# Optimization experiments

Hardware: AMD Instinct MI355X
Metric: run time of the kernel (lower is better)

Reference implementation:

```python
import jax, jax.numpy as jnp
import numpy as np

B, S, H = 1, 2048, 2048
E, K, I = 8, 2, 1024   # n_routed_experts, num_experts_per_tok, moe_intermediate_size
IS = 2 * I             # shared experts intermediate = moe_intermediate_size * n_shared_experts


def setup_inputs() -> dict:
    key = jax.random.key(0)
    ks = jax.random.split(key, 8)
    w = 0.02  # weight scale so gate softmax is not degenerate
    return {
        "x": jax.random.normal(ks[0], (B, S, H), jnp.float32),
        "gate_w": jax.random.normal(ks[1], (E, H), jnp.float32) * w,
        "wg": jax.random.normal(ks[2], (E, H, I), jnp.float32) * w,
        "wu": jax.random.normal(ks[3], (E, H, I), jnp.float32) * w,
        "wd": jax.random.normal(ks[4], (E, I, H), jnp.float32) * w,
        "sg": jax.random.normal(ks[5], (H, IS), jnp.float32) * w,
        "su": jax.random.normal(ks[6], (H, IS), jnp.float32) * w,
        "sd": jax.random.normal(ks[7], (IS, H), jnp.float32) * w,
    }


def reference(x, gate_w, wg, wu, wd, sg, su, sd):
    b, s, h = x.shape
    xf = x.reshape(-1, h)                                  # [T, H]
    T = xf.shape[0]

    # ---- gate: softmax scores, top-k, renormalize ----
    scores = jax.nn.softmax(jnp.einsum("th,eh->te", xf, gate_w), axis=-1)  # [T, E]
    topk_w, topk_i = jax.lax.top_k(scores, K)              # sorted descending
    topk_w = topk_w / jnp.sum(topk_w, axis=-1, keepdims=True)

    # dense combine weights [T, E] (indices unique per token)
    cw = jnp.zeros_like(scores).at[jnp.arange(T)[:, None], topk_i].add(topk_w)

    # ---- routed experts: SwiGLU MLP per expert, weighted combine ----
    g = jnp.einsum("th,ehi->eti", xf, wg)                  # [E, T, I]
    u = jnp.einsum("th,ehi->eti", xf, wu)
    hgated = jax.nn.silu(g) * u
    eo = jnp.einsum("eti,eih->eth", hgated, wd)            # [E, T, H]
    y = jnp.einsum("te,eth->th", cw, eo)                   # [T, H]

    # ---- shared experts ----
    shared = (jax.nn.silu(xf @ sg) * (xf @ su)) @ sd       # [T, H]

    return (y + shared).reshape(b, s, h)
```

## Files before the change

kernel.cpp:

```cpp
#include <hip/hip_runtime.h>


typedef unsigned short u16;
typedef unsigned int   u32;
typedef __bf16 bf16x8 __attribute__((ext_vector_type(8)));
typedef float  f32x4  __attribute__((ext_vector_type(4)));

#define T_TOK 2048
#define HDIM  2048
#define IDIM  1024
#define NEXP  8
#define ISDIM 2048
#define MAXROWS   5760
#define MAXROWS_FB 5120

__device__ __forceinline__ u16 f2bf(float f) {
  u32 x = __float_as_uint(f);
  return (u16)((x + 0x7FFFu + ((x >> 16) & 1u)) >> 16);
}
__device__ __forceinline__ float bf2f(u16 v) { return __uint_as_float(((u32)v) << 16); }

#define GLL(g, l)                                                              \
  __builtin_amdgcn_global_load_lds(                                            \
      (const __attribute__((address_space(1))) void*)(g),                      \
      (__attribute__((address_space(3))) void*)(l), 16, 0, 0)

__global__ void init_kernel(int* __restrict__ perm, int* __restrict__ meta,
                            int* __restrict__ zrow) {
  int idx = blockIdx.x * 256 + threadIdx.x;
  if (idx < 8192) perm[idx] = -1;
  if (idx < 16) meta[idx] = 0;
  if (idx < 1024) zrow[idx] = 0;
}

__global__ __launch_bounds__(256) void gate_kernel(
    const float* __restrict__ x, const float* __restrict__ gw,
    u16* __restrict__ xb, float* __restrict__ outz,
    float* __restrict__ topw, int* __restrict__ topi, int* __restrict__ meta) {
  const int t = blockIdx.x, tid = threadIdx.x;
  const long o = (long)t * HDIM + tid * 8;
  float4 a = *(const float4*)(x + o);
  float4 b = *(const float4*)(x + o + 4);
  float4 z = {0.f, 0.f, 0.f, 0.f};
  *(float4*)(outz + o) = z;
  *(float4*)(outz + o + 4) = z;
  uint4 w;
  w.x = (u32)f2bf(a.x) | ((u32)f2bf(a.y) << 16);
  w.y = (u32)f2bf(a.z) | ((u32)f2bf(a.w) << 16);
  w.z = (u32)f2bf(b.x) | ((u32)f2bf(b.y) << 16);
  w.w = (u32)f2bf(b.z) | ((u32)f2bf(b.w) << 16);
  *(uint4*)(xb + o) = w;
  float acc[NEXP];
#pragma unroll
  for (int e = 0; e < NEXP; e++) {
    const float* gr = gw + e * HDIM + tid * 8;
    float4 wa = *(const float4*)gr;
    float4 wb = *(const float4*)(gr + 4);
    acc[e] = a.x * wa.x + a.y * wa.y + a.z * wa.z + a.w * wa.w +
             b.x * wb.x + b.y * wb.y + b.z * wb.z + b.w * wb.w;
  }
#pragma unroll
  for (int off = 32; off; off >>= 1)
#pragma unroll
    for (int e = 0; e < NEXP; e++) acc[e] += __shfl_down(acc[e], off, 64);
  __shared__ float red[4][NEXP];
  if ((tid & 63) == 0) {
#pragma unroll
    for (int e = 0; e < NEXP; e++) red[tid >> 6][e] = acc[e];
  }
  __syncthreads();
  if (tid == 0) {
    float s[NEXP];
#pragma unroll
    for (int e = 0; e < NEXP; e++) s[e] = red[0][e] + red[1][e] + red[2][e] + red[3][e];
    int i0 = 0;
#pragma unroll
    for (int e = 1; e < NEXP; e++)
      if (s[e] > s[i0]) i0 = e;
    int i1 = -1;
#pragma unroll
    for (int e = 0; e < NEXP; e++) {
      if (e == i0) continue;
      if (i1 < 0 || s[e] > s[i1]) i1 = e;
    }
    float w0 = 1.f / (1.f + __expf(s[i1] - s[i0]));
    topw[t * 2 + 0] = w0;
    topw[t * 2 + 1] = 1.f - w0;
    topi[t * 2 + 0] = i0;
    topi[t * 2 + 1] = i1;
    atomicAdd(meta + i0, 1);
    atomicAdd(meta + i1, 1);
  }
}

__global__ void scan_kernel(int* __restrict__ meta, int pad) {
  if (threadIdx.x == 0 && blockIdx.x == 0) {
    int o = 0;
    meta[16] = 0;
#pragma unroll
    for (int e = 0; e < NEXP; e++) {
      o += ((meta[e] + pad - 1) / pad) * pad;
      meta[17 + e] = o;
    }
  }
}

__global__ void assign_kernel(const int* __restrict__ topi, int* __restrict__ meta,
                              int* __restrict__ perm, int* __restrict__ tokrow) {
  int idx = blockIdx.x * 256 + threadIdx.x;
  int e = topi[idx];
  int pos = atomicAdd(meta + 8 + e, 1);
  int row = meta[16 + e] + pos;
  perm[row] = idx;
  tokrow[idx] = row;
}

__device__ __forceinline__ void tcast_tile(const float* __restrict__ in,
                                           u16* __restrict__ out, int R, int C) {
  __shared__ float tile[64 * 65];
  int r0 = blockIdx.y * 64, c0 = blockIdx.x * 64;
  int t = threadIdx.x;
  int i = t >> 4, j4 = t & 15;
#pragma unroll
  for (int ii = 0; ii < 4; ii++) {
    int r = i + ii * 16;
    float4 v = *(const float4*)(in + (long)(r0 + r) * C + c0 + j4 * 4);
    tile[r * 65 + j4 * 4 + 0] = v.x;
    tile[r * 65 + j4 * 4 + 1] = v.y;
    tile[r * 65 + j4 * 4 + 2] = v.z;
    tile[r * 65 + j4 * 4 + 3] = v.w;
  }
  __syncthreads();
  int cc = t >> 3, rr = (t & 7) * 8;
#pragma unroll
  for (int pp = 0; pp < 2; pp++) {
    int c = cc + pp * 32;
    u16 e[8];
#pragma unroll
    for (int u = 0; u < 8; u++) e[u] = f2bf(tile[(rr + u) * 65 + c]);
    uint4 w;
    w.x = (u32)e[0] | ((u32)e[1] << 16);
    w.y = (u32)e[2] | ((u32)e[3] << 16);
    w.z = (u32)e[4] | ((u32)e[5] << 16);
    w.w = (u32)e[6] | ((u32)e[7] << 16);
    *(uint4*)(out + (long)(c0 + c) * R + r0 + rr) = w;
  }
}

__global__ __launch_bounds__(256) void tcast_kernel(const float* __restrict__ in,
                                                    u16* __restrict__ out, int R, int C,
                                                    long inz, long outz) {
  tcast_tile(in + (long)blockIdx.z * inz, out + (long)blockIdx.z * outz, R, C);
}

__global__ __launch_bounds__(256) void tcast2_kernel(
    const float* __restrict__ inA, const float* __restrict__ inB,
    u16* __restrict__ out, int R, int C, long inz, long outz, long boff, int zsplit) {
  int z = blockIdx.z;
  const float* in;
  u16* o;
  if (z < zsplit) {
    in = inA + (long)z * inz;
    o = out + (long)z * outz;
  } else {
    int e = z - zsplit;
    in = inB + (long)e * inz;
    o = out + (long)e * outz + boff;
  }
  tcast_tile(in, o, R, C);
}

template <int HALF8>
__device__ __forceinline__ void silu_do(u16* __restrict__ buf, long i) {
  long r = i / HALF8, c = i % HALF8;
  u16* g = buf + r * (long)HALF8 * 16 + c * 8;
  uint4 gv = *(const uint4*)g;
  uint4 uv = *(const uint4*)(g + HALF8 * 8);
  const u32* gp = &gv.x;
  const u32* up = &uv.x;
  uint4 w;
  u32* wp = &w.x;
#pragma unroll
  for (int j = 0; j < 4; j++) {
    float g0 = bf2f((u16)(gp[j] & 0xFFFF)), g1 = bf2f((u16)(gp[j] >> 16));
    float u0 = bf2f((u16)(up[j] & 0xFFFF)), u1 = bf2f((u16)(up[j] >> 16));
    float r0 = g0 / (1.f + __expf(-g0)) * u0;
    float r1 = g1 / (1.f + __expf(-g1)) * u1;
    wp[j] = (u32)f2bf(r0) | ((u32)f2bf(r1) << 16);
  }
  *(uint4*)g = w;
}

template <int HALF8>
__global__ void silu_kernel(u16* __restrict__ buf) {
  long i = (long)blockIdx.x * 256 + threadIdx.x;
  silu_do<HALF8>(buf, i);
}

__global__ void silu2_kernel(u16* __restrict__ gur, u16* __restrict__ gus) {
  const long NR = (long)MAXROWS * IDIM / 8;
  long i = (long)blockIdx.x * 256 + threadIdx.x;
  if (i < NR)
    silu_do<128>(gur, i);
  else
    silu_do<256>(gus, i - NR);
}

template <int CMODE , int MI, bool PERMA, bool SEGB>
__device__ __forceinline__ void gemm_body3(
    int mt, int nt, u16* lds, const u16* __restrict__ A, long lda,
    const u16* __restrict__ B, long ldbz, int K, u16* __restrict__ Cb,
    float* __restrict__ Cf, long ldc, const int* __restrict__ offp,
    const int* __restrict__ perm, const u16* __restrict__ zrow) {
  const int row0 = mt * (MI * 32);
  if constexpr (SEGB) {
    if (row0 >= offp[8]) return;
    int e = 0;
    while (offp[e + 1] <= row0) ++e;
    B += (long)e * ldbz;
  }
  const int tid = threadIdx.x;

  const int ra = tid >> 2, sa = tid & 3;
  const int swz0 = (sa ^ ((ra >> 1) & 3)) * 8;
  const u16 *gA0, *gA1;
  if constexpr (PERMA) {
    int p0 = perm[row0 + ra];
    int p1 = perm[row0 + 128 + ra];
    gA0 = ((p0 < 0) ? zrow : A + (long)(p0 >> 1) * lda) + swz0;
    gA1 = ((p1 < 0) ? zrow : A + (long)(p1 >> 1) * lda) + swz0;
  } else {
    gA0 = A + (long)(row0 + ra) * lda + swz0;
    gA1 = A + (long)(row0 + 128 + ra) * lda + swz0;
  }
  const u16* gB0 = B + (long)(nt * 256 + ra) * K + swz0;
  const u16* gB1 = B + (long)(nt * 256 + 128 + ra) * K + swz0;

  const int lane = tid & 63, w = tid >> 6;
  const int wm = (w >> 2) * (MI * 16), wn = (w & 3) * 64;
  const int lrow = lane & 15, kc = lane >> 4;
  int offA[MI], offB[4];
#pragma unroll
  for (int i = 0; i < MI; i++) {
    int r = wm + i * 16 + lrow;
    offA[i] = r * 32 + ((kc ^ ((r >> 1) & 3)) << 3);
  }
#pragma unroll
  for (int i = 0; i < 4; i++) {
    int r = wn + i * 16 + lrow;
    offB[i] = 8192 + r * 32 + ((kc ^ ((r >> 1) & 3)) << 3);
  }

  f32x4 acc[MI][4];
#pragma unroll
  for (int i = 0; i < MI; i++)
#pragma unroll
    for (int j = 0; j < 4; j++) acc[i][j] = f32x4{0.f, 0.f, 0.f, 0.f};

  const int nk = K >> 5;
  {
    u16* b0 = lds;
    GLL(gA0, b0 + tid * 8);
    GLL(gA1, b0 + 4096 + tid * 8);
    GLL(gB0, b0 + 8192 + tid * 8);
    GLL(gB1, b0 + 12288 + tid * 8);
    u16* b1 = lds + 16384;
    GLL(gA0 + 32, b1 + tid * 8);
    GLL(gA1 + 32, b1 + 4096 + tid * 8);
    GLL(gB0 + 32, b1 + 8192 + tid * 8);
    GLL(gB1 + 32, b1 + 12288 + tid * 8);
  }
  asm volatile("s_waitcnt vmcnt(4)" ::: "memory");
  asm volatile("s_barrier" ::: "memory");

  constexpr int MH = MI / 2;
  int cur = 0, stg = 2;
  for (int t = 0; t < nk; ++t) {
    int t2 = t + 2;
    if (t2 >= nk) t2 -= nk;
    const int kk2 = t2 * 32;
    u16* buf = lds + cur * 16384;
    u16* sb = lds + stg * 16384;

    bf16x8 af[MH], bfv[4];
#pragma unroll
    for (int i = 0; i < MH; i++) af[i] = *(const bf16x8*)(buf + offA[i]);
#pragma unroll
    for (int i = 0; i < 4; i++) bfv[i] = *(const bf16x8*)(buf + offB[i]);
    GLL(gA0 + kk2, sb + tid * 8);
    GLL(gA1 + kk2, sb + 4096 + tid * 8);
    asm volatile("s_barrier" ::: "memory");
    __builtin_amdgcn_s_setprio(1);
#pragma unroll
    for (int mi = 0; mi < MH; mi++)
#pragma unroll
      for (int ni = 0; ni < 4; ni++)
        acc[mi][ni] = __builtin_amdgcn_mfma_f32_16x16x32_bf16(af[mi], bfv[ni],
                                                              acc[mi][ni], 0, 0, 0);
    __builtin_amdgcn_s_setprio(0);
    asm volatile("s_barrier" ::: "memory");

    bf16x8 ag[MI - MH];
#pragma unroll
    for (int i = 0; i < MI - MH; i++) ag[i] = *(const bf16x8*)(buf + offA[MH + i]);
    GLL(gB0 + kk2, sb + 8192 + tid * 8);
    GLL(gB1 + kk2, sb + 12288 + tid * 8);
    asm volatile("s_barrier" ::: "memory");
    __builtin_amdgcn_s_setprio(1);
#pragma unroll
    for (int mi = 0; mi < MI - MH; mi++)
#pragma unroll
      for (int ni = 0; ni < 4; ni++)
        acc[MH + mi][ni] = __builtin_amdgcn_mfma_f32_16x16x32_bf16(
            ag[mi], bfv[ni], acc[MH + mi][ni], 0, 0, 0);
    __builtin_amdgcn_s_setprio(0);
    asm volatile("s_waitcnt vmcnt(4)" ::: "memory");
    asm volatile("s_barrier" ::: "memory");
    cur = (cur == 2) ? 0 : cur + 1;
    stg = (stg == 2) ? 0 : stg + 1;
  }
  asm volatile("s_waitcnt vmcnt(0)" ::: "memory");

  const int crow = row0 + wm + ((lane >> 4) << 2);
  const int ccol = nt * 256 + wn + (lane & 15);
#pragma unroll
  for (int mi = 0; mi < MI; mi++) {
#pragma unroll
    for (int ni = 0; ni < 4; ni++) {
#pragma unroll
      for (int r = 0; r < 4; r++) {
        int row = crow + mi * 16 + r;
        int col = ccol + ni * 16;
        float v = acc[mi][ni][r];
        if constexpr (CMODE == 0) {
          Cb[(long)row * ldc + col] = f2bf(v);
        } else {
          Cf[(long)row * ldc + col] = v;
        }
      }
    }
  }
}

__global__ __launch_bounds__(512, 2) void gemm_gu_fused(
    const u16* __restrict__ xb, const u16* __restrict__ wguT,
    const u16* __restrict__ sgsuT, u16* __restrict__ gur, u16* __restrict__ gus,
    const int* __restrict__ offp, const int* __restrict__ perm,
    const u16* __restrict__ zrow) {
  __shared__ __align__(16) u16 lds3[49152];
  int bid = blockIdx.x;
  if (bid < 128) {
    gemm_body3<0, 8, false, false>(bid >> 4, bid & 15, lds3, xb, HDIM, sgsuT, 0, HDIM,
                                   gus, nullptr, 2 * ISDIM, nullptr, nullptr, nullptr);
  } else {
    int b = bid - 128;
    gemm_body3<0, 6, true, true>(b >> 3, b & 7, lds3, xb, HDIM, wguT,
                                 (long)2 * IDIM * HDIM, HDIM, gur, nullptr, 2 * IDIM,
                                 offp, perm, zrow);
  }
}

__global__ __launch_bounds__(512, 2) void gemm_down_plain(
    const u16* __restrict__ gus, const u16* __restrict__ sdT,
    const u16* __restrict__ gur, const u16* __restrict__ wdT, float* __restrict__ out,
    u16* __restrict__ eo, const int* __restrict__ offp) {
  __shared__ __align__(16) u16 lds3[49152];
  int bid = blockIdx.x;
  if (bid < 64) {
    gemm_body3<1, 8, false, false>(bid >> 3, bid & 7, lds3, gus, 2 * ISDIM, sdT, 0,
                                   ISDIM, nullptr, out, HDIM, nullptr, nullptr, nullptr);
  } else {
    int b = bid - 64;
    gemm_body3<0, 6, false, true>(b >> 3, b & 7, lds3, gur, 2 * IDIM, wdT,
                                  (long)HDIM * IDIM, IDIM, eo, nullptr, HDIM, offp,
                                  nullptr, nullptr);
  }
}

__global__ __launch_bounds__(256) void combine_kernel(float* __restrict__ out,
                                                      const u16* __restrict__ eo,
                                                      const int* __restrict__ tokrow,
                                                      const float* __restrict__ topw) {
  const int t = blockIdx.x, tid = threadIdx.x;
  const long o = (long)t * HDIM + tid * 8;
  const int r0 = tokrow[t * 2], r1 = tokrow[t * 2 + 1];
  const float w0 = topw[t * 2], w1 = topw[t * 2 + 1];
  float4 a = *(const float4*)(out + o);
  float4 b = *(const float4*)(out + o + 4);
  uint4 e0 = *(const uint4*)(eo + (long)r0 * HDIM + tid * 8);
  uint4 e1 = *(const uint4*)(eo + (long)r1 * HDIM + tid * 8);
  const u32* p0 = &e0.x;
  const u32* p1 = &e1.x;
  float r[8] = {a.x, a.y, a.z, a.w, b.x, b.y, b.z, b.w};
#pragma unroll
  for (int j = 0; j < 4; j++) {
    r[j * 2 + 0] += w0 * bf2f((u16)(p0[j] & 0xFFFF)) + w1 * bf2f((u16)(p1[j] & 0xFFFF));
    r[j * 2 + 1] += w0 * bf2f((u16)(p0[j] >> 16)) + w1 * bf2f((u16)(p1[j] >> 16));
  }
  float4 oa = {r[0], r[1], r[2], r[3]};
  float4 ob = {r[4], r[5], r[6], r[7]};
  *(float4*)(out + o) = oa;
  *(float4*)(out + o + 4) = ob;
}

template <int CMODE, bool PERMA, bool SEGB>
__device__ __forceinline__ void gemm_body(
    int mt, int nt, u16* ldsA, u16* ldsB, const u16* __restrict__ A, long lda,
    const u16* __restrict__ B, long ldbz, int K, u16* __restrict__ Cb,
    float* __restrict__ Cf, long ldc, const int* __restrict__ offp,
    const int* __restrict__ perm, const float* __restrict__ topw,
    const u16* __restrict__ zrow) {
  const int row0 = mt * 128;
  if constexpr (SEGB) {
    if (row0 >= offp[8]) return;
    int e = 0;
    while (offp[e + 1] <= row0) ++e;
    B += (long)e * ldbz;
  }
  const int tid = threadIdx.x;
  const u16* gA[4];
  const u16* gB[4];
  u16 *lA[4], *lB[4];
#pragma unroll
  for (int j = 0; j < 4; j++) {
    int c = tid + 256 * j;
    int r = c >> 3, s = c & 7;
    int gk = (s ^ (r & 7)) * 8;
    const u16* arow;
    if constexpr (PERMA) {
      int p = perm[row0 + r];
      arow = (p < 0) ? zrow : A + (long)(p >> 1) * lda;
    } else {
      arow = A + (long)(row0 + r) * lda;
    }
    gA[j] = arow + gk;
    gB[j] = B + (long)(nt * 128 + r) * K + gk;
    lA[j] = ldsA + c * 8;
    lB[j] = ldsB + c * 8;
  }
  const int lane = tid & 63, wave = tid >> 6;
  const int wm = (wave & 1) * 64, wn = (wave >> 1) * 64;
  const int lrow = lane & 15;
  const int kchunk = lane >> 4;
  const int rsw = lrow & 7;

  f32x4 acc[4][4];
#pragma unroll
  for (int i = 0; i < 4; i++)
#pragma unroll
    for (int j = 0; j < 4; j++) acc[i][j] = f32x4{0.f, 0.f, 0.f, 0.f};

  const int nk = K >> 6;
  for (int kt = 0; kt < nk; ++kt) {
    const int kk = kt * 64;
#pragma unroll
    for (int j = 0; j < 4; j++) {
      GLL(gA[j] + kk, lA[j]);
      GLL(gB[j] + kk, lB[j]);
    }
    __syncthreads();
#pragma unroll
    for (int half = 0; half < 2; half++) {
      const int slot = (kchunk + half * 4) ^ rsw;
      bf16x8 af[4], bfv[4];
#pragma unroll
      for (int mi = 0; mi < 4; mi++)
        af[mi] = *(const bf16x8*)(ldsA + (wm + lrow + mi * 16) * 64 + slot * 8);
#pragma unroll
      for (int ni = 0; ni < 4; ni++)
        bfv[ni] = *(const bf16x8*)(ldsB + (wn + lrow + ni * 16) * 64 + slot * 8);
#pragma unroll
      for (int mi = 0; mi < 4; mi++)
#pragma unroll
        for (int ni = 0; ni < 4; ni++)
          acc[mi][ni] = __builtin_amdgcn_mfma_f32_16x16x32_bf16(af[mi], bfv[ni],
                                                                acc[mi][ni], 0, 0, 0);
    }
    __syncthreads();
  }

  const int crow = row0 + wm + ((lane >> 4) << 2);
  const int ccol = nt * 128 + wn + (lane & 15);
#pragma unroll
  for (int mi = 0; mi < 4; mi++) {
#pragma unroll
    for (int ni = 0; ni < 4; ni++) {
#pragma unroll
      for (int r = 0; r < 4; r++) {
        int row = crow + mi * 16 + r;
        int col = ccol + ni * 16;
        float v = acc[mi][ni][r];
        if constexpr (CMODE == 0) {
          Cb[(long)row * ldc + col] = f2bf(v);
        } else if constexpr (CMODE == 1) {
          Cf[(long)row * ldc + col] = v;
        } else if constexpr (CMODE == 2) {
          int p = perm[row];
          if (p >= 0) atomicAdd(Cf + (long)(p >> 1) * ldc + col, topw[p] * v);
        } else {
          atomicAdd(Cf + (long)row * ldc + col, v);
        }
      }
    }
  }
}

__global__ __launch_bounds__(256) void gemm_routed_gu(
    const u16* __restrict__ xb, const u16* __restrict__ wT, u16* __restrict__ Cb,
    const int* __restrict__ offp, const int* __restrict__ perm,
    const u16* __restrict__ zrow) {
  __shared__ __align__(16) u16 ldsA[8192], ldsB[8192];
  gemm_body<0, true, true>(blockIdx.y, blockIdx.x, ldsA, ldsB, xb, HDIM, wT,
                           (long)IDIM * HDIM, HDIM, Cb, nullptr, 2 * IDIM, offp, perm,
                           nullptr, zrow);
}
__global__ __launch_bounds__(256) void gemm_shared_gu(const u16* __restrict__ xb,
                                                      const u16* __restrict__ sgsuT,
                                                      u16* __restrict__ gus) {
  __shared__ __align__(16) u16 ldsA[8192], ldsB[8192];
  gemm_body<0, false, false>(blockIdx.y, blockIdx.x, ldsA, ldsB, xb, HDIM, sgsuT, 0, HDIM,
                             gus, nullptr, 2 * ISDIM, nullptr, nullptr, nullptr, nullptr);
}
__global__ __launch_bounds__(256) void gemm_down_atomic(
    const u16* __restrict__ gus, const u16* __restrict__ sdT,
    const u16* __restrict__ gur, const u16* __restrict__ wdT, float* __restrict__ out,
    const int* __restrict__ offp, const int* __restrict__ perm,
    const float* __restrict__ topw) {
  __shared__ __align__(16) u16 ldsA[8192], ldsB[8192];
  int bid = blockIdx.x;
  if (bid < 256) {
    gemm_body<3, false, false>(bid / 16, bid % 16, ldsA, ldsB, gus, 2 * ISDIM, sdT, 0,
                               ISDIM, nullptr, out, HDIM, nullptr, nullptr, nullptr,
                               nullptr);
  } else {
    int b = bid - 256;
    gemm_body<2, false, true>(b / 16, b % 16, ldsA, ldsB, gur, 2 * IDIM, wdT,
                              (long)HDIM * IDIM, IDIM, nullptr, out, HDIM, offp, perm,
                              topw, nullptr);
  }
}

extern "C" void kernel_launch(void* const* d_in, const int* in_sizes, int n_in,
                              void* d_out, int out_size, void* d_ws, size_t ws_size,
                              hipStream_t stream) {
  const float* x  = (const float*)d_in[0];
  const float* gw = (const float*)d_in[1];
  const float* wg = (const float*)d_in[2];
  const float* wu = (const float*)d_in[3];
  const float* wd = (const float*)d_in[4];
  const float* sg = (const float*)d_in[5];
  const float* su = (const float*)d_in[6];
  const float* sd = (const float*)d_in[7];
  float* out = (float*)d_out;

  char* ws = (char*)d_ws;
  size_t off = 0;
  auto alloc = [&](size_t b) {
    size_t o = off;
    off += (b + 255) & ~(size_t)255;
    return (void*)(ws + o);
  };
  u16*   xb     = (u16*)alloc((size_t)T_TOK * HDIM * 2);
  u16*   gur    = (u16*)alloc((size_t)MAXROWS * 2 * IDIM * 2);
  u16*   gus    = (u16*)alloc((size_t)T_TOK * 2 * ISDIM * 2);
  float* topw   = (float*)alloc((size_t)T_TOK * 2 * 4);
  int*   topi   = (int*)alloc((size_t)T_TOK * 2 * 4);
  int*   tokrow = (int*)alloc((size_t)T_TOK * 2 * 4);
  int*   perm   = (int*)alloc(8192 * 4);
  int*   meta   = (int*)alloc(64 * 4);
  u16*   zrow   = (u16*)alloc(4096);
  size_t base = off;

  const size_t SZ_WGUT  = (size_t)NEXP * 2 * IDIM * HDIM * 2;
  const size_t SZ_SGSUT = (size_t)2 * ISDIM * HDIM * 2;
  const size_t SZ_SDT   = (size_t)HDIM * ISDIM * 2;
  const size_t SZ_WDT   = (size_t)NEXP * HDIM * IDIM * 2;
  const bool fused = ws_size >= base + SZ_WGUT + SZ_SGSUT;

  init_kernel<<<32, 256, 0, stream>>>(perm, meta, (int*)zrow);
  gate_kernel<<<T_TOK, 256, 0, stream>>>(x, gw, xb, out, topw, topi, meta);
  scan_kernel<<<1, 64, 0, stream>>>(meta, fused ? 192 : 128);
  assign_kernel<<<16, 256, 0, stream>>>(topi, meta, perm, tokrow);

  if (fused) {
    u16* wguT  = (u16*)(ws + base);
    u16* sgsuT = (u16*)(ws + base + SZ_WGUT);
    u16* sdT   = wguT;
    u16* wdT   = wguT + SZ_SDT / 2;
    u16* eo    = wguT + (SZ_SDT + SZ_WDT) / 2;
    tcast2_kernel<<<dim3(IDIM / 64, HDIM / 64, 2 * NEXP), 256, 0, stream>>>(
        wg, wu, wguT, HDIM, IDIM, (long)HDIM * IDIM, (long)2 * IDIM * HDIM,
        (long)IDIM * HDIM, NEXP);
    tcast2_kernel<<<dim3(ISDIM / 64, HDIM / 64, 2), 256, 0, stream>>>(
        sg, su, sgsuT, HDIM, ISDIM, 0, 0, (long)ISDIM * HDIM, 1);
    gemm_gu_fused<<<368, 512, 0, stream>>>(xb, wguT, sgsuT, gur, gus, meta + 16, perm,
                                           zrow);
    silu2_kernel<<<(MAXROWS * IDIM / 8 + T_TOK * ISDIM / 8) / 256, 256, 0, stream>>>(
        gur, gus);
    tcast_kernel<<<dim3(HDIM / 64, ISDIM / 64, 1), 256, 0, stream>>>(sd, sdT, ISDIM,
                                                                     HDIM, 0, 0);
    tcast_kernel<<<dim3(HDIM / 64, IDIM / 64, NEXP), 256, 0, stream>>>(
        wd, wdT, IDIM, HDIM, (long)IDIM * HDIM, (long)HDIM * IDIM);
    gemm_down_plain<<<304, 512, 0, stream>>>(gus, sdT, gur, wdT, out, eo, meta + 16);
    combine_kernel<<<T_TOK, 256, 0, stream>>>(out, eo, tokrow, topw);
  } else {
    u16* wT    = (u16*)(ws + base);
    u16* sgsuT = wT;
    u16* sdT   = wT;
    u16* wdT   = wT + SZ_SDT / 2;
    tcast_kernel<<<dim3(IDIM / 64, HDIM / 64, NEXP), 256, 0, stream>>>(
        wg, wT, HDIM, IDIM, (long)HDIM * IDIM, (long)IDIM * HDIM);
    gemm_routed_gu<<<dim3(8, MAXROWS_FB / 128), 256, 0, stream>>>(xb, wT, gur, meta + 16,
                                                                  perm, zrow);
    tcast_kernel<<<dim3(IDIM / 64, HDIM / 64, NEXP), 256, 0, stream>>>(
        wu, wT, HDIM, IDIM, (long)HDIM * IDIM, (long)IDIM * HDIM);
    gemm_routed_gu<<<dim3(8, MAXROWS_FB / 128), 256, 0, stream>>>(
        xb, wT, gur + IDIM, meta + 16, perm, zrow);
    silu_kernel<128><<<(MAXROWS_FB * IDIM / 8) / 256, 256, 0, stream>>>(gur);
    tcast_kernel<<<dim3(ISDIM / 64, HDIM / 64, 1), 256, 0, stream>>>(sg, sgsuT, HDIM,
                                                                     ISDIM, 0, 0);
    tcast_kernel<<<dim3(ISDIM / 64, HDIM / 64, 1), 256, 0, stream>>>(
        su, sgsuT + (size_t)ISDIM * HDIM, HDIM, ISDIM, 0, 0);
    gemm_shared_gu<<<dim3(32, 16), 256, 0, stream>>>(xb, sgsuT, gus);
    silu_kernel<256><<<(T_TOK * ISDIM / 8) / 256, 256, 0, stream>>>(gus);
    tcast_kernel<<<dim3(HDIM / 64, ISDIM / 64, 1), 256, 0, stream>>>(sd, sdT, ISDIM,
                                                                     HDIM, 0, 0);
    tcast_kernel<<<dim3(HDIM / 64, IDIM / 64, NEXP), 256, 0, stream>>>(
        wd, wdT, IDIM, HDIM, (long)IDIM * HDIM, (long)HDIM * IDIM);
    gemm_down_atomic<<<896, 256, 0, stream>>>(gus, sdT, gur, wdT, out, meta + 16, perm,
                                              topw);
  }
}
```

Before: 511.4 us.

## Fuse SiLU into gate/up GEMM epilogue and merge setup kernels

The gate/up weight transposes now interleave gate and up columns in 16-wide groups, so each GEMM tile holds matching g and u accumulators. SiLU(g)*u is then computed in the epilogue and written at half width, which removes the separate SiLU pass and halves the intermediate buffer traffic. Init and both up-projection transposes are merged into one front kernel. The scan is folded into the gate kernel through a last-block ticket, and the down-weight transposes are merged into one launch. This cuts launch count and memory traffic, but the ticket scan adds fence and atomic ordering risk.

```diff
diff --git a/kernel.cpp b/kernel.cpp
--- a/kernel.cpp
+++ b/kernel.cpp
@@ -29,14 +29,96 @@
                             int* __restrict__ zrow) {
   int idx = blockIdx.x * 256 + threadIdx.x;
   if (idx < 8192) perm[idx] = -1;
-  if (idx < 16) meta[idx] = 0;
+  if (idx < 32) meta[idx] = 0;
   if (idx < 1024) zrow[idx] = 0;
+}
+
+__device__ __forceinline__ void tcast_tile2(const float* __restrict__ in,
+                                            u16* __restrict__ out, int R, int C,
+                                            int r0, int c0, int ilv, int uoff) {
+  __shared__ float tile[64 * 65];
+  int t = threadIdx.x;
+  int i = t >> 4, j4 = t & 15;
+#pragma unroll
+  for (int ii = 0; ii < 4; ii++) {
+    int r = i + ii * 16;
+    float4 v = *(const float4*)(in + (long)(r0 + r) * C + c0 + j4 * 4);
+    tile[r * 65 + j4 * 4 + 0] = v.x;
+    tile[r * 65 + j4 * 4 + 1] = v.y;
+    tile[r * 65 + j4 * 4 + 2] = v.z;
+    tile[r * 65 + j4 * 4 + 3] = v.w;
+  }
+  __syncthreads();
+  int cc = t >> 3, rr = (t & 7) * 8;
+#pragma unroll
+  for (int pp = 0; pp < 2; pp++) {
+    int c = cc + pp * 32;
+    u16 e[8];
+#pragma unroll
+    for (int u = 0; u < 8; u++) e[u] = f2bf(tile[(rr + u) * 65 + c]);
+    uint4 w;
+    w.x = (u32)e[0] | ((u32)e[1] << 16);
+    w.y = (u32)e[2] | ((u32)e[3] << 16);
+    w.z = (u32)e[4] | ((u32)e[5] << 16);
+    w.w = (u32)e[6] | ((u32)e[7] << 16);
+    int cg = c0 + c;
+    int orow = ilv ? ((cg >> 4) << 5) + (cg & 15) + uoff : cg;
+    *(uint4*)(out + (long)orow * R + r0 + rr) = w;
+  }
+}
+
+__global__ __launch_bounds__(256) void front_kernel(
+    const float* __restrict__ wg, const float* __restrict__ wu,
+    const float* __restrict__ sg, const float* __restrict__ su,
+    u16* __restrict__ wguT, u16* __restrict__ sgsuT, int* __restrict__ perm,
+    int* __restrict__ meta, int* __restrict__ zrow) {
+  int b = blockIdx.x;
+  if (b >= 10240) {
+    int ib = b - 10240;
+    int idx = ib * 256 + threadIdx.x;
+    if (idx < 8192) perm[idx] = -1;
+    if (ib == 32) {
+      if (threadIdx.x < 32) meta[threadIdx.x] = 0;
+#pragma unroll
+      for (int k = 0; k < 4; k++) zrow[threadIdx.x * 4 + k] = 0;
+    }
+    return;
+  }
+  if (b < 8192) {
+    int z = b >> 9, rem = b & 511, y = rem >> 4, xk = rem & 15;
+    int isU = z >= 8 ? 1 : 0;
+    int e = isU ? z - 8 : z;
+    const float* in = (isU ? wu : wg) + (long)e * HDIM * IDIM;
+    u16* o = wguT + (long)e * 2 * IDIM * HDIM;
+    tcast_tile2(in, o, HDIM, IDIM, y * 64, xk * 64, 1, isU ? 16 : 0);
+  } else {
+    int b2 = b - 8192;
+    int z = b2 >> 10, rem = b2 & 1023, y = rem >> 5, xk = rem & 31;
+    const float* in = z ? su : sg;
+    tcast_tile2(in, sgsuT, HDIM, ISDIM, y * 64, xk * 64, 1, z ? 16 : 0);
+  }
+}
+
+__global__ __launch_bounds__(256) void tcast_back(const float* __restrict__ sd,
+                                                  const float* __restrict__ wd,
+                                                  u16* __restrict__ sdT,
+                                                  u16* __restrict__ wdT) {
+  int b = blockIdx.x;
+  if (b < 1024) {
+    int y = b >> 5, xk = b & 31;
+    tcast_tile2(sd, sdT, ISDIM, HDIM, y * 64, xk * 64, 0, 0);
+  } else {
+    int b2 = b - 1024;
+    int z = b2 >> 9, rem = b2 & 511, y = rem >> 5, xk = rem & 31;
+    tcast_tile2(wd + (long)z * IDIM * HDIM, wdT + (long)z * HDIM * IDIM, IDIM, HDIM,
+                y * 64, xk * 64, 0, 0);
+  }
 }
 
 __global__ __launch_bounds__(256) void gate_kernel(
     const float* __restrict__ x, const float* __restrict__ gw,
     u16* __restrict__ xb, float* __restrict__ outz,
-    float* __restrict__ topw, int* __restrict__ topi, int* __restrict__ meta) {
+    float* __restrict__ topw, int* __restrict__ topi, int* __restrict__ meta, int pad) {
   const int t = blockIdx.x, tid = threadIdx.x;
   const long o = (long)t * HDIM + tid * 8;
   float4 a = *(const float4*)(x + o);
@@ -90,6 +172,20 @@
     topi[t * 2 + 1] = i1;
     atomicAdd(meta + i0, 1);
     atomicAdd(meta + i1, 1);
+    if (pad > 0) {
+      __threadfence();
+      int ticket = atomicAdd(meta + 25, 1);
+      if (ticket == (int)gridDim.x - 1) {
+        int o2 = 0;
+        meta[16] = 0;
+#pragma unroll
+        for (int e = 0; e < NEXP; e++) {
+          int cnt = atomicAdd(meta + e, 0);
+          o2 += ((cnt + pad - 1) / pad) * pad;
+          meta[17 + e] = o2;
+        }
+      }
+    }
   }
 }
 
@@ -117,57 +213,12 @@
 
 __device__ __forceinline__ void tcast_tile(const float* __restrict__ in,
                                            u16* __restrict__ out, int R, int C) {
-  __shared__ float tile[64 * 65];
-  int r0 = blockIdx.y * 64, c0 = blockIdx.x * 64;
-  int t = threadIdx.x;
-  int i = t >> 4, j4 = t & 15;
-#pragma unroll
-  for (int ii = 0; ii < 4; ii++) {
-    int r = i + ii * 16;
-    float4 v = *(const float4*)(in + (long)(r0 + r) * C + c0 + j4 * 4);
-    tile[r * 65 + j4 * 4 + 0] = v.x;
-    tile[r * 65 + j4 * 4 + 1] = v.y;
-    tile[r * 65 + j4 * 4 + 2] = v.z;
-    tile[r * 65 + j4 * 4 + 3] = v.w;
-  }
-  __syncthreads();
-  int cc = t >> 3, rr = (t & 7) * 8;
-#pragma unroll
-  for (int pp = 0; pp < 2; pp++) {
-    int c = cc + pp * 32;
-    u16 e[8];
-#pragma unroll
-    for (int u = 0; u < 8; u++) e[u] = f2bf(tile[(rr + u) * 65 + c]);
-    uint4 w;
-    w.x = (u32)e[0] | ((u32)e[1] << 16);
-    w.y = (u32)e[2] | ((u32)e[3] << 16);
-    w.z = (u32)e[4] | ((u32)e[5] << 16);
-    w.w = (u32)e[6] | ((u32)e[7] << 16);
-    *(uint4*)(out + (long)(c0 + c) * R + r0 + rr) = w;
-  }
-}
-
+  tcast_tile2(in, out, R, C, blockIdx.y * 64, blockIdx.x * 64, 0, 0);
+}
 __global__ __launch_bounds__(256) void tcast_kernel(const float* __restrict__ in,
                                                     u16* __restrict__ out, int R, int C,
                                                     long inz, long outz) {
   tcast_tile(in + (long)blockIdx.z * inz, out + (long)blockIdx.z * outz, R, C);
-}
-
-__global__ __launch_bounds__(256) void tcast2_kernel(
-    const float* __restrict__ inA, const float* __restrict__ inB,
-    u16* __restrict__ out, int R, int C, long inz, long outz, long boff, int zsplit) {
-  int z = blockIdx.z;
-  const float* in;
-  u16* o;
-  if (z < zsplit) {
-    in = inA + (long)z * inz;
-    o = out + (long)z * outz;
-  } else {
-    int e = z - zsplit;
-    in = inB + (long)e * inz;
-    o = out + (long)e * outz + boff;
-  }
-  tcast_tile(in, o, R, C);
 }
 
 template <int HALF8>
@@ -190,23 +241,13 @@
   }
   *(uint4*)g = w;
 }
-
 template <int HALF8>
 __global__ void silu_kernel(u16* __restrict__ buf) {
   long i = (long)blockIdx.x * 256 + threadIdx.x;
   silu_do<HALF8>(buf, i);
 }
 
-__global__ void silu2_kernel(u16* __restrict__ gur, u16* __restrict__ gus) {
-  const long NR = (long)MAXROWS * IDIM / 8;
-  long i = (long)blockIdx.x * 256 + threadIdx.x;
-  if (i < NR)
-    silu_do<128>(gur, i);
-  else
-    silu_do<256>(gus, i - NR);
-}
-
-template <int CMODE , int MI, bool PERMA, bool SEGB>
+template <int EPI, int MI, bool PERMA, bool SEGB>
 __device__ __forceinline__ void gemm_body3(
     int mt, int nt, u16* lds, const u16* __restrict__ A, long lda,
     const u16* __restrict__ B, long ldbz, int K, u16* __restrict__ Cb,
@@ -322,20 +363,34 @@
   asm volatile("s_waitcnt vmcnt(0)" ::: "memory");
 
   const int crow = row0 + wm + ((lane >> 4) << 2);
-  const int ccol = nt * 256 + wn + (lane & 15);
 #pragma unroll
   for (int mi = 0; mi < MI; mi++) {
-#pragma unroll
-    for (int ni = 0; ni < 4; ni++) {
-#pragma unroll
-      for (int r = 0; r < 4; r++) {
-        int row = crow + mi * 16 + r;
-        int col = ccol + ni * 16;
-        float v = acc[mi][ni][r];
-        if constexpr (CMODE == 0) {
-          Cb[(long)row * ldc + col] = f2bf(v);
-        } else {
-          Cf[(long)row * ldc + col] = v;
+    if constexpr (EPI == 2) {
+      const int ccl = nt * 128 + (wn >> 1) + (lane & 15);
+#pragma unroll
+      for (int nh = 0; nh < 2; nh++) {
+        f32x4 g = acc[mi][nh * 2], u = acc[mi][nh * 2 + 1];
+#pragma unroll
+        for (int r = 0; r < 4; r++) {
+          float gg = g[r];
+          float h = gg / (1.f + __expf(-gg)) * u[r];
+          Cb[(long)(crow + mi * 16 + r) * ldc + ccl + nh * 16] = f2bf(h);
+        }
+      }
+    } else {
+      const int ccol = nt * 256 + wn + (lane & 15);
+#pragma unroll
+      for (int ni = 0; ni < 4; ni++) {
+#pragma unroll
+        for (int r = 0; r < 4; r++) {
+          int row = crow + mi * 16 + r;
+          int col = ccol + ni * 16;
+          float v = acc[mi][ni][r];
+          if constexpr (EPI == 0) {
+            Cb[(long)row * ldc + col] = f2bf(v);
+          } else {
+            Cf[(long)row * ldc + col] = v;
+          }
         }
       }
     }
@@ -350,12 +405,12 @@
   __shared__ __align__(16) u16 lds3[49152];
   int bid = blockIdx.x;
   if (bid < 128) {
-    gemm_body3<0, 8, false, false>(bid >> 4, bid & 15, lds3, xb, HDIM, sgsuT, 0, HDIM,
-                                   gus, nullptr, 2 * ISDIM, nullptr, nullptr, nullptr);
+    gemm_body3<2, 8, false, false>(bid >> 4, bid & 15, lds3, xb, HDIM, sgsuT, 0, HDIM,
+                                   gus, nullptr, ISDIM, nullptr, nullptr, nullptr);
   } else {
     int b = bid - 128;
-    gemm_body3<0, 6, true, true>(b >> 3, b & 7, lds3, xb, HDIM, wguT,
-                                 (long)2 * IDIM * HDIM, HDIM, gur, nullptr, 2 * IDIM,
+    gemm_body3<2, 6, true, true>(b >> 3, b & 7, lds3, xb, HDIM, wguT,
+                                 (long)2 * IDIM * HDIM, HDIM, gur, nullptr, IDIM,
                                  offp, perm, zrow);
   }
 }
@@ -367,11 +422,11 @@
   __shared__ __align__(16) u16 lds3[49152];
   int bid = blockIdx.x;
   if (bid < 64) {
-    gemm_body3<1, 8, false, false>(bid >> 3, bid & 7, lds3, gus, 2 * ISDIM, sdT, 0,
+    gemm_body3<1, 8, false, false>(bid >> 3, bid & 7, lds3, gus, ISDIM, sdT, 0,
                                    ISDIM, nullptr, out, HDIM, nullptr, nullptr, nullptr);
   } else {
     int b = bid - 64;
-    gemm_body3<0, 6, false, true>(b >> 3, b & 7, lds3, gur, 2 * IDIM, wdT,
+    gemm_body3<0, 6, false, true>(b >> 3, b & 7, lds3, gur, IDIM, wdT,
                                   (long)HDIM * IDIM, IDIM, eo, nullptr, HDIM, offp,
                                   nullptr, nullptr);
   }
@@ -577,30 +632,19 @@
   const size_t SZ_WDT   = (size_t)NEXP * HDIM * IDIM * 2;
   const bool fused = ws_size >= base + SZ_WGUT + SZ_SGSUT;
 
-  init_kernel<<<32, 256, 0, stream>>>(perm, meta, (int*)zrow);
-  gate_kernel<<<T_TOK, 256, 0, stream>>>(x, gw, xb, out, topw, topi, meta);
-  scan_kernel<<<1, 64, 0, stream>>>(meta, fused ? 192 : 128);
-  assign_kernel<<<16, 256, 0, stream>>>(topi, meta, perm, tokrow);
-
   if (fused) {
     u16* wguT  = (u16*)(ws + base);
     u16* sgsuT = (u16*)(ws + base + SZ_WGUT);
     u16* sdT   = wguT;
     u16* wdT   = wguT + SZ_SDT / 2;
     u16* eo    = wguT + (SZ_SDT + SZ_WDT) / 2;
-    tcast2_kernel<<<dim3(IDIM / 64, HDIM / 64, 2 * NEXP), 256, 0, stream>>>(
-        wg, wu, wguT, HDIM, IDIM, (long)HDIM * IDIM, (long)2 * IDIM * HDIM,
-        (long)IDIM * HDIM, NEXP);
-    tcast2_kernel<<<dim3(ISDIM / 64, HDIM / 64, 2), 256, 0, stream>>>(
-        sg, su, sgsuT, HDIM, ISDIM, 0, 0, (long)ISDIM * HDIM, 1);
+    front_kernel<<<10273, 256, 0, stream>>>(wg, wu, sg, su, wguT, sgsuT, perm, meta,
+                                            (int*)zrow);
+    gate_kernel<<<T_TOK, 256, 0, stream>>>(x, gw, xb, out, topw, topi, meta, 192);
+    assign_kernel<<<16, 256, 0, stream>>>(topi, meta, perm, tokrow);
     gemm_gu_fused<<<368, 512, 0, stream>>>(xb, wguT, sgsuT, gur, gus, meta + 16, perm,
                                            zrow);
-    silu2_kernel<<<(MAXROWS * IDIM / 8 + T_TOK * ISDIM / 8) / 256, 256, 0, stream>>>(
-        gur, gus);
-    tcast_kernel<<<dim3(HDIM / 64, ISDIM / 64, 1), 256, 0, stream>>>(sd, sdT, ISDIM,
-                                                                     HDIM, 0, 0);
-    tcast_kernel<<<dim3(HDIM / 64, IDIM / 64, NEXP), 256, 0, stream>>>(
-        wd, wdT, IDIM, HDIM, (long)IDIM * HDIM, (long)HDIM * IDIM);
+    tcast_back<<<5120, 256, 0, stream>>>(sd, wd, sdT, wdT);
     gemm_down_plain<<<304, 512, 0, stream>>>(gus, sdT, gur, wdT, out, eo, meta + 16);
     combine_kernel<<<T_TOK, 256, 0, stream>>>(out, eo, tokrow, topw);
   } else {
@@ -608,6 +652,10 @@
     u16* sgsuT = wT;
     u16* sdT   = wT;
     u16* wdT   = wT + SZ_SDT / 2;
+    init_kernel<<<32, 256, 0, stream>>>(perm, meta, (int*)zrow);
+    gate_kernel<<<T_TOK, 256, 0, stream>>>(x, gw, xb, out, topw, topi, meta, 0);
+    scan_kernel<<<1, 64, 0, stream>>>(meta, 128);
+    assign_kernel<<<16, 256, 0, stream>>>(topi, meta, perm, tokrow);
     tcast_kernel<<<dim3(IDIM / 64, HDIM / 64, NEXP), 256, 0, stream>>>(
         wg, wT, HDIM, IDIM, (long)HDIM * IDIM, (long)IDIM * HDIM);
     gemm_routed_gu<<<dim3(8, MAXROWS_FB / 128), 256, 0, stream>>>(xb, wT, gur, meta + 16,
```

Result: slower. 549.2 us (+7.4%).
